# Kernel tuning notes

Hardware: AMD Instinct MI355X
Metric: run time of the kernel (lower is better)

The kernel has to match this reference:

```python
import jax, jax.numpy as jnp
import numpy as np

V, E, H, B, S, T = 32000, 32, 128, 128, 512, 16


def _gru_cell(x, h, w_ih, w_hh, b_ih, b_hh):
    # PyTorch GRU cell semantics.  x: [B, in], h: [B, H]
    gi = x @ w_ih.T + b_ih              # [B, 3H]
    gh = h @ w_hh.T + b_hh              # [B, 3H]
    i_r, i_z, i_n = jnp.split(gi, 3, axis=-1)
    h_r, h_z, h_n = jnp.split(gh, 3, axis=-1)
    r = jax.nn.sigmoid(i_r + h_r)
    z = jax.nn.sigmoid(i_z + h_z)
    n = jnp.tanh(i_n + r * h_n)
    return (1.0 - z) * n + z * h


def setup_inputs() -> dict:
    key = jax.random.key(0)
    ks = jax.random.split(key, 24)
    Hh = H // 2  # encoder hidden per direction = 64
    u = lambda k, shp, fan: jax.random.uniform(k, shp, jnp.float32, -1.0, 1.0) / np.sqrt(fan)
    inp = {
        'inputs': jax.random.randint(ks[0], (B, S), 0, V),
        'targets': jax.random.randint(ks[1], (B, T), 0, V),
        'emb': jax.random.normal(ks[2], (V, E), jnp.float32),
        # encoder forward direction
        'W_ih_f': u(ks[3], (3 * Hh, E), Hh), 'W_hh_f': u(ks[4], (3 * Hh, Hh), Hh),
        'b_ih_f': u(ks[5], (3 * Hh,), Hh), 'b_hh_f': u(ks[6], (3 * Hh,), Hh),
        # encoder backward direction
        'W_ih_b': u(ks[7], (3 * Hh, E), Hh), 'W_hh_b': u(ks[8], (3 * Hh, Hh), Hh),
        'b_ih_b': u(ks[9], (3 * Hh,), Hh), 'b_hh_b': u(ks[10], (3 * Hh,), Hh),
        # sGate linears
        'W1': u(ks[11], (H, H), H), 'b1': u(ks[12], (H,), H),
        'W2': u(ks[13], (H, H), H), 'b2': u(ks[14], (H,), H),
        # decoder GRU (input E + H = 160, hidden H)
        'W_ih_d': u(ks[15], (3 * H, E + H), H), 'W_hh_d': u(ks[16], (3 * H, H), H),
        'b_ih_d': u(ks[17], (3 * H,), H), 'b_hh_d': u(ks[18], (3 * H,), H),
        # decoder2vocab
        'W_out': u(ks[19], (V, H), H), 'b_out': u(ks[20], (V,), H),
    }
    return inp


def reference(inputs, targets, emb, W_ih_f, W_hh_f, b_ih_f, b_hh_f,
              W_ih_b, W_hh_b, b_ih_b, b_hh_b, W1, b1, W2, b2,
              W_ih_d, W_hh_d, b_ih_d, b_hh_d, W_out, b_out):
    Hh = H // 2
    # ---- encode ----
    embeds = emb[inputs]                       # [B, S, E]
    xs = embeds.transpose(1, 0, 2)             # [S, B, E] time-major
    h0 = jnp.zeros((inputs.shape[0], Hh), jnp.float32)

    def fwd_step(h, x):
        h = _gru_cell(x, h, W_ih_f, W_hh_f, b_ih_f, b_hh_f)
        return h, h

    def bwd_step(h, x):
        h = _gru_cell(x, h, W_ih_b, W_hh_b, b_ih_b, b_hh_b)
        return h, h

    h_f, outs_f = jax.lax.scan(fwd_step, h0, xs)
    h_b, outs_b = jax.lax.scan(bwd_step, h0, xs[::-1])
    outs_b = outs_b[::-1]
    outputs = jnp.concatenate([outs_f, outs_b], axis=-1).transpose(1, 0, 2)  # [B, S, H]
    sn = jnp.concatenate([h_f, h_b], axis=-1)[:, None, :]                    # [B, 1, H]
    sGate = jax.nn.sigmoid(outputs @ W1.T + b1 + sn @ W2.T + b2)
    enc_outs = outputs * sGate                                               # [B, S, H]

    # ---- attention decode (teacher forcing) ----
    h_dec0 = sn[:, 0, :]                       # [B, H]
    words = targets[:, :-1].T                  # [T-1, B]

    def dec_step(h, w):
        e = emb[w]                                                  # [B, E]
        alpha = jax.nn.softmax(jnp.einsum('bd,bsd->bs', h, enc_outs))
        c_t = jnp.einsum('bs,bsd->bd', alpha, enc_outs)             # [B, H]
        h = _gru_cell(jnp.concatenate([c_t, e], axis=-1), h,
                      W_ih_d, W_hh_d, b_ih_d, b_hh_d)
        return h, h @ W_out.T + b_out

    _, logits = jax.lax.scan(dec_step, h_dec0, words)  # [T-1, B, V]
    return logits.transpose(1, 0, 2)                   # [B, T-1, V]
```

## Files before the change

kernel.cpp:

```cpp
#include <hip/hip_runtime.h>
#include <hip/hip_bf16.h>


typedef unsigned short u16;
typedef unsigned int u32;
typedef __attribute__((ext_vector_type(8))) short short8;
typedef __attribute__((ext_vector_type(4))) float f32x4;

#define V_ 32000
#define E_ 32
#define H_ 128
#define B_ 128
#define S_ 512
#define TDEC 15

__device__ __forceinline__ float bfu(u32 u) {
    union { u32 i; float f; } v; v.i = u << 16; return v.f;
}
__device__ __forceinline__ u16 f2bf(float f) {
    union { float f; u32 i; } v; v.f = f;
    u32 x = v.i;
    u32 r = (x + 0x7fffu + ((x >> 16) & 1u)) >> 16;
    return (u16)r;
}
__device__ __forceinline__ void bf8_to_f(const uint4 p, float* f) {
    f[0] = bfu(p.x & 0xffffu); f[1] = bfu(p.x >> 16);
    f[2] = bfu(p.y & 0xffffu); f[3] = bfu(p.y >> 16);
    f[4] = bfu(p.z & 0xffffu); f[5] = bfu(p.z >> 16);
    f[6] = bfu(p.w & 0xffffu); f[7] = bfu(p.w >> 16);
}
__device__ __forceinline__ float sigm(float x) { return 1.f / (1.f + expf(-x)); }
__device__ __forceinline__ float sigm_fast(float x) { return 1.f / (1.f + __expf(-x)); }
__device__ __forceinline__ float tanh_fast(float x) {
    const float t = __expf(2.f * x);
    return (t - 1.f) / (t + 1.f);
}

__global__ __launch_bounds__(384) void gi_kernel(
    const int* __restrict__ inputs, const float* __restrict__ emb,
    const float* __restrict__ Wih_f, const float* __restrict__ bih_f,
    const float* __restrict__ bhh_f,
    const float* __restrict__ Wih_b, const float* __restrict__ bih_b,
    const float* __restrict__ bhh_b,
    float* __restrict__ gi)
{
    const int b  = blockIdx.x >> 3;
    const int s0 = (blockIdx.x & 7) << 6;
    const int tid = threadIdx.x;

    __shared__ float xs[64][E_];
    __shared__ int idx[64];
    if (tid < 64) idx[tid] = inputs[b * S_ + s0 + tid];
    __syncthreads();
    for (int i = tid; i < 64 * E_; i += 384) {
        xs[i >> 5][i & 31] = emb[(unsigned)idx[i >> 5] * E_ + (i & 31)];
    }
    __syncthreads();

    const int dir = (tid >= 192) ? 1 : 0;
    const int j = tid - dir * 192;
    const float* Wih = dir ? Wih_b : Wih_f;
    const float* bih = dir ? bih_b : bih_f;
    const float* bhh = dir ? bhh_b : bhh_f;

    float w[E_];
    #pragma unroll
    for (int k = 0; k < E_; k += 4)
        *(float4*)(w + k) = *(const float4*)(Wih + j * E_ + k);
    const float c = bih[j] + (j < 128 ? bhh[j] : 0.f);

    float* gout = gi + (((size_t)(dir * B_ + b)) * S_ + s0) * 192 + j;
    for (int r = 0; r < 64; r++) {
        const float4* xr = (const float4*)xs[r];
        float a0 = 0.f, a1 = 0.f, a2 = 0.f, a3 = 0.f;
        #pragma unroll
        for (int q = 0; q < E_ / 4; q++) {
            const float4 x = xr[q];
            a0 += x.x * w[4 * q + 0]; a1 += x.y * w[4 * q + 1];
            a2 += x.z * w[4 * q + 2]; a3 += x.w * w[4 * q + 3];
        }
        gout[(size_t)r * 192] = ((a0 + a1) + (a2 + a3)) + c;
    }
}

__global__ __launch_bounds__(192, 1) void encoder_kernel(
    const float* __restrict__ gi,
    const float* __restrict__ Whh_f, const float* __restrict__ bhh_f,
    const float* __restrict__ Whh_b, const float* __restrict__ bhh_b,
    u16* __restrict__ outputs, float* __restrict__ sn)
{
    const int tid = threadIdx.x;
    const int g = tid >> 6;
    const int j = tid & 63;
    const int b = blockIdx.x & 127;
    const int dir = blockIdx.x >> 7;

    const float* Whh = dir ? Whh_b : Whh_f;
    const float* bhh = dir ? bhh_b : bhh_f;

    f32x4 wv[16];
    {
        const f32x4* wr = (const f32x4*)(Whh + (g * 64 + j) * 64);
        #pragma unroll
        for (int k = 0; k < 16; k++) wv[k] = wr[k];
    }
    const float badd = (g == 2) ? bhh[128 + j] : 0.f;

    __shared__ __attribute__((aligned(16))) float hs[64];
    __shared__ float sg[4 * 64];
    if (tid < 64) hs[tid] = 0.f;
    float hmine = 0.f;

    const float* gp = gi + ((size_t)(dir * B_ + b)) * S_ * 192 + g * 64 + j;
    u16* orow = outputs + ((size_t)b * S_) * H_ + (dir << 6) + j;

    const int st = dir ? -1 : 1;
    int oc = dir ? (S_ - 1) : 0;

    float pa = gp[(long)oc * 192];
    float pb = gp[(long)(oc + st) * 192];

#define ENC_STEP(PCUR)                                                         \
    {                                                                          \
        __syncthreads();                  \
        f32x4 acc = {0.f, 0.f, 0.f, 0.f};                                      \
        _Pragma("unroll")                                                      \
        for (int q = 0; q < 16; q++)                                           \
            acc += *(const f32x4*)(hs + 4 * q) * wv[q];                        \
        const float d = (acc[0] + acc[1]) + (acc[2] + acc[3]);                 \
        if (g == 2) { sg[128 + j] = d + badd; sg[192 + j] = PCUR; }            \
        else        { sg[g * 64 + j] = d + PCUR; }                             \
        PCUR = gp[(long)(oc + 2 * st) * 192];           \
        __syncthreads();                                         \
        if (g == 0) {                                                          \
            const float r = sigm_fast(sg[j]);                                  \
            const float z = sigm_fast(sg[64 + j]);                             \
            const float n = tanh_fast(sg[192 + j] + r * sg[128 + j]);          \
            const float hn = n + z * (hmine - n);                              \
            hmine = hn;                                                        \
            hs[j] = hn;                                                        \
            orow[(long)oc * H_] = f2bf(hn);                                    \
        }                                                                      \
        oc += st;                                                              \
    }

    for (int s = 0; s < S_; s += 2) {
        ENC_STEP(pa)
        ENC_STEP(pb)
    }
#undef ENC_STEP

    if (g == 0) sn[(b << 7) + (dir << 6) + j] = hmine;
}

__global__ __launch_bounds__(128) void t2_kernel(
    const float* __restrict__ sn, const float* __restrict__ W2,
    const float* __restrict__ b2, float* __restrict__ t2)
{
    const int b = blockIdx.x, h = threadIdx.x;
    __shared__ float s_[H_];
    s_[h] = sn[b * H_ + h];
    __syncthreads();
    const float4* wr = (const float4*)(W2 + h * H_);
    float a0 = 0.f, a1 = 0.f, a2 = 0.f, a3 = 0.f;
    #pragma unroll 4
    for (int k = 0; k < H_ / 4; k++) {
        const float4 p = wr[k];
        a0 += s_[4 * k + 0] * p.x; a1 += s_[4 * k + 1] * p.y;
        a2 += s_[4 * k + 2] * p.z; a3 += s_[4 * k + 3] * p.w;
    }
    t2[b * H_ + h] = ((a0 + a1) + (a2 + a3)) + b2[h];
}

__global__ __launch_bounds__(256) void cvt_bf16_kernel(
    const float* __restrict__ src, u16* __restrict__ dst)
{
    const int i = (blockIdx.x * 256 + threadIdx.x) * 4;
    const float4 p = *(const float4*)(src + i);
    ushort4 q;
    q.x = f2bf(p.x); q.y = f2bf(p.y); q.z = f2bf(p.z); q.w = f2bf(p.w);
    *(ushort4*)(dst + i) = q;
}

__global__ __launch_bounds__(256) void gate_mfma_kernel(
    const u16* __restrict__ outputs, const u16* __restrict__ W1b,
    const float* __restrict__ b1, const float* __restrict__ t2,
    u16* __restrict__ enc)
{
    const int l = threadIdx.x & 63;
    const int w = threadIdx.x >> 6;
    const int tile_m = blockIdx.x * 64 + w * 16;
    const int row_a = tile_m + (l & 15);
    const int kb = (l >> 4) * 8;
    const int b = blockIdx.x >> 3;

    f32x4 acc[8] = {};
    #pragma unroll
    for (int kk = 0; kk < 4; kk++) {
        const int k0 = kk * 32 + kb;
        const short8 af = *(const short8*)(outputs + row_a * H_ + k0);
        #pragma unroll
        for (int i = 0; i < 8; i++) {
            const int n = i * 16 + (l & 15);
            const short8 bv = *(const short8*)(W1b + n * H_ + k0);
            acc[i] = __builtin_amdgcn_mfma_f32_16x16x32_bf16(af, bv, acc[i], 0, 0, 0);
        }
    }

    const int m_base = tile_m + (l >> 4) * 4;
    #pragma unroll
    for (int i = 0; i < 8; i++) {
        const int n = i * 16 + (l & 15);
        const float bias = b1[n] + t2[b * H_ + n];
        #pragma unroll
        for (int r = 0; r < 4; r++) {
            const int m = m_base + r;
            const float g = sigm_fast(acc[i][r] + bias);
            const float o = bfu(outputs[m * H_ + n]);
            enc[m * H_ + n] = f2bf(o * g);
        }
    }
}

__global__ __launch_bounds__(512) void decoder_kernel(
    const int* __restrict__ targets, const float* __restrict__ emb,
    const float* __restrict__ Wihd, const float* __restrict__ Whhd,
    const float* __restrict__ bihd, const float* __restrict__ bhhd,
    const u16* __restrict__ enc, const float* __restrict__ sn,
    u16* __restrict__ h_all)
{
    const int b = blockIdx.x;
    const int tid = threadIdx.x;
    const int lane = tid & 63;
    const int wid = tid >> 6;

    __shared__ __attribute__((aligned(16))) float h[H_];
    __shared__ float sc[S_];
    __shared__ float xv[H_ + E_];
    __shared__ float redm[8], reds[8];
    __shared__ float cpart[4][H_];
    __shared__ float sgi[3 * H_];
    __shared__ float sgh[3 * H_];

    if (tid < H_) h[tid] = sn[b * H_ + tid];
    __syncthreads();

    const u16* encb = enc + b * S_ * H_;

    for (int t = 0; t < TDEC; t++) {
        const int word = targets[b * 16 + t];

        const u16* row = encb + tid * H_;
        float a0 = 0.f, a1 = 0.f, a2 = 0.f, a3 = 0.f;
        #pragma unroll
        for (int k = 0; k < H_; k += 8) {
            uint4 p = *(const uint4*)(row + k);
            float f[8]; bf8_to_f(p, f);
            const f32x4 h0 = *(const f32x4*)(h + k);
            const f32x4 h1 = *(const f32x4*)(h + k + 4);
            a0 += h0[0] * f[0]; a1 += h0[1] * f[1];
            a2 += h0[2] * f[2]; a3 += h0[3] * f[3];
            a0 += h1[0] * f[4]; a1 += h1[1] * f[5];
            a2 += h1[2] * f[6]; a3 += h1[3] * f[7];
        }
        const float d = (a0 + a1) + (a2 + a3);

        float m = d;
        #pragma unroll
        for (int off = 32; off > 0; off >>= 1) m = fmaxf(m, __shfl_xor(m, off));
        if (lane == 0) redm[wid] = m;
        __syncthreads();
        float bm = redm[0];
        #pragma unroll
        for (int i = 1; i < 8; i++) bm = fmaxf(bm, redm[i]);
        const float e = expf(d - bm);
        float ssum = e;
        #pragma unroll
        for (int off = 32; off > 0; off >>= 1) ssum += __shfl_xor(ssum, off);
        if (lane == 0) reds[wid] = ssum;
        __syncthreads();
        float tot = reds[0];
        #pragma unroll
        for (int i = 1; i < 8; i++) tot += reds[i];
        sc[tid] = e * (1.f / tot);
        __syncthreads();

        {
            const int k = tid & 127;
            const int q = tid >> 7;
            const u16* basep = encb + (q * 128) * H_ + k;
            const float* al = sc + q * 128;
            float c0 = 0.f, c1 = 0.f, c2 = 0.f, c3 = 0.f;
            #pragma unroll 8
            for (int s = 0; s < 128; s += 4) {
                c0 += al[s + 0] * bfu(basep[(s + 0) * H_]);
                c1 += al[s + 1] * bfu(basep[(s + 1) * H_]);
                c2 += al[s + 2] * bfu(basep[(s + 2) * H_]);
                c3 += al[s + 3] * bfu(basep[(s + 3) * H_]);
            }
            cpart[q][k] = (c0 + c1) + (c2 + c3);
        }
        __syncthreads();
        if (tid < H_) xv[tid] = (cpart[0][tid] + cpart[1][tid]) + (cpart[2][tid] + cpart[3][tid]);
        else if (tid < H_ + E_) xv[tid] = emb[(unsigned)word * E_ + (tid - H_)];
        __syncthreads();

        if (tid < 3 * H_) {
            const int j = tid;
            const float4* wr = (const float4*)(Wihd + j * (H_ + E_));
            float g0 = 0.f, g1 = 0.f, g2 = 0.f, g3 = 0.f;
            #pragma unroll 8
            for (int k = 0; k < (H_ + E_) / 4; k++) {
                const float4 p = wr[k];
                g0 += xv[4 * k + 0] * p.x; g1 += xv[4 * k + 1] * p.y;
                g2 += xv[4 * k + 2] * p.z; g3 += xv[4 * k + 3] * p.w;
            }
            sgi[j] = ((g0 + g1) + (g2 + g3)) + bihd[j];

            const float4* hr = (const float4*)(Whhd + j * H_);
            float b0 = 0.f, b1_ = 0.f, b2_ = 0.f, b3 = 0.f;
            #pragma unroll 8
            for (int k = 0; k < H_ / 4; k++) {
                const float4 p = hr[k];
                b0  += h[4 * k + 0] * p.x; b1_ += h[4 * k + 1] * p.y;
                b2_ += h[4 * k + 2] * p.z; b3  += h[4 * k + 3] * p.w;
            }
            sgh[j] = ((b0 + b1_) + (b2_ + b3)) + bhhd[j];
        }
        __syncthreads();

        if (tid < H_) {
            const float r = sigm(sgi[tid] + sgh[tid]);
            const float z = sigm(sgi[H_ + tid] + sgh[H_ + tid]);
            const float n = tanhf(sgi[2 * H_ + tid] + r * sgh[2 * H_ + tid]);
            const float hn = (1.f - z) * n + z * h[tid];
            h[tid] = hn;
            h_all[(t * B_ + b) * H_ + tid] = f2bf(hn);
        }
        __syncthreads();
    }
}

__global__ __launch_bounds__(256) void logits_kernel(
    const u16* __restrict__ hall, const u16* __restrict__ Woutb,
    const float* __restrict__ bout, float* __restrict__ out)
{
    const int l = threadIdx.x & 63;
    const int w = threadIdx.x >> 6;
    const int tile_n = blockIdx.x * 64;
    const int tile_m = blockIdx.y * 64 + w * 16;

    f32x4 acc[4] = {};
    const int row_a = tile_m + (l & 15);
    const int kb = (l >> 4) * 8;

    #pragma unroll
    for (int kk = 0; kk < 4; kk++) {
        const int k0 = kk * 32 + kb;
        const short8 af = *(const short8*)(hall + row_a * H_ + k0);
        #pragma unroll
        for (int i = 0; i < 4; i++) {
            const int n = tile_n + i * 16 + (l & 15);
            const short8 bv = *(const short8*)(Woutb + n * H_ + k0);
            acc[i] = __builtin_amdgcn_mfma_f32_16x16x32_bf16(af, bv, acc[i], 0, 0, 0);
        }
    }

    const int m_base = tile_m + (l >> 4) * 4;
    #pragma unroll
    for (int i = 0; i < 4; i++) {
        const int n = tile_n + i * 16 + (l & 15);
        const float bias = bout[n];
        #pragma unroll
        for (int r = 0; r < 4; r++) {
            const int m = m_base + r;
            const int t = m >> 7;
            const int bb = m & 127;
            out[(size_t)(bb * TDEC + t) * V_ + n] = acc[i][r] + bias;
        }
    }
}

extern "C" void kernel_launch(void* const* d_in, const int* in_sizes, int n_in,
                              void* d_out, int out_size, void* d_ws, size_t ws_size,
                              hipStream_t stream) {
    const int*   inputs  = (const int*)d_in[0];
    const int*   targets = (const int*)d_in[1];
    const float* emb     = (const float*)d_in[2];
    const float* Wih_f   = (const float*)d_in[3];
    const float* Whh_f   = (const float*)d_in[4];
    const float* bih_f   = (const float*)d_in[5];
    const float* bhh_f   = (const float*)d_in[6];
    const float* Wih_b   = (const float*)d_in[7];
    const float* Whh_b   = (const float*)d_in[8];
    const float* bih_b   = (const float*)d_in[9];
    const float* bhh_b   = (const float*)d_in[10];
    const float* W1      = (const float*)d_in[11];
    const float* b1      = (const float*)d_in[12];
    const float* W2      = (const float*)d_in[13];
    const float* b2      = (const float*)d_in[14];
    const float* Wihd    = (const float*)d_in[15];
    const float* Whhd    = (const float*)d_in[16];
    const float* bihd    = (const float*)d_in[17];
    const float* bhhd    = (const float*)d_in[18];
    const float* Wout    = (const float*)d_in[19];
    const float* bout    = (const float*)d_in[20];
    float* out = (float*)d_out;

    u16*   outputs = (u16*)d_out;
    u16*   enc     = (u16*)((char*)d_out + 16777216);
    u16*   W1b     = (u16*)((char*)d_out + 33554432);
    float* gi      = (float*)((char*)d_out + 33619968);

    char* ws = (char*)d_ws;
    float* sn    = (float*)(ws);
    float* t2    = (float*)(ws + 65536);
    u16*   h_all = (u16*)(ws + 131072);
    u16*   Woutb = (u16*)(ws + 622592);

    gi_kernel<<<B_ * (S_ / 64), 384, 0, stream>>>(inputs, emb, Wih_f, bih_f, bhh_f,
                                                  Wih_b, bih_b, bhh_b, gi);
    encoder_kernel<<<256, 192, 0, stream>>>(gi, Whh_f, bhh_f, Whh_b, bhh_b, outputs, sn);
    t2_kernel<<<128, 128, 0, stream>>>(sn, W2, b2, t2);
    cvt_bf16_kernel<<<H_ * H_ / 1024, 256, 0, stream>>>(W1, W1b);
    cvt_bf16_kernel<<<V_ * H_ / 1024, 256, 0, stream>>>(Wout, Woutb);
    gate_mfma_kernel<<<B_ * S_ / 64, 256, 0, stream>>>(outputs, W1b, b1, t2, enc);
    decoder_kernel<<<128, 512, 0, stream>>>(targets, emb, Wihd, Whhd, bihd, bhhd,
                                            enc, sn, h_all);
    logits_kernel<<<dim3(500, 30), 256, 0, stream>>>(h_all, Woutb, bout, out);
}
```

Baseline: 972.0 us.

## Stage per-batch encoder outputs in swizzled LDS for decoder attention

```diff
diff --git a/kernel.cpp b/kernel.cpp
--- a/kernel.cpp
+++ b/kernel.cpp
@@ -222,7 +222,7 @@
     }
 }
 
-__global__ __launch_bounds__(512) void decoder_kernel(
+__global__ __launch_bounds__(512, 1) void decoder_kernel(
     const int* __restrict__ targets, const float* __restrict__ emb,
     const float* __restrict__ Wihd, const float* __restrict__ Whhd,
     const float* __restrict__ bihd, const float* __restrict__ bhhd,
@@ -234,36 +234,51 @@
     const int lane = tid & 63;
     const int wid = tid >> 6;
 
+    __shared__ __attribute__((aligned(16))) u16 enc_lds[S_ * H_];
     __shared__ __attribute__((aligned(16))) float h[H_];
     __shared__ float sc[S_];
     __shared__ float xv[H_ + E_];
     __shared__ float redm[8], reds[8];
-    __shared__ float cpart[4][H_];
+    __shared__ __attribute__((aligned(16))) float cpart[32][H_];
     __shared__ float sgi[3 * H_];
     __shared__ float sgh[3 * H_];
 
+    const u16* encb = enc + b * S_ * H_;
+
+    {
+        const int c = tid & 15;
+        const int sb = tid >> 4;
+        #pragma unroll
+        for (int i = 0; i < 16; i++) {
+            const int s = i * 32 + sb;
+            const uint4 p = *(const uint4*)(encb + s * H_ + c * 8);
+            *(uint4*)(enc_lds + s * H_ + ((c ^ (s & 15)) * 8)) = p;
+        }
+    }
     if (tid < H_) h[tid] = sn[b * H_ + tid];
     __syncthreads();
 
-    const u16* encb = enc + b * S_ * H_;
-
     for (int t = 0; t < TDEC; t++) {
         const int word = targets[b * 16 + t];
 
-        const u16* row = encb + tid * H_;
-        float a0 = 0.f, a1 = 0.f, a2 = 0.f, a3 = 0.f;
-        #pragma unroll
-        for (int k = 0; k < H_; k += 8) {
-            uint4 p = *(const uint4*)(row + k);
-            float f[8]; bf8_to_f(p, f);
-            const f32x4 h0 = *(const f32x4*)(h + k);
-            const f32x4 h1 = *(const f32x4*)(h + k + 4);
-            a0 += h0[0] * f[0]; a1 += h0[1] * f[1];
-            a2 += h0[2] * f[2]; a3 += h0[3] * f[3];
-            a0 += h1[0] * f[4]; a1 += h1[1] * f[5];
-            a2 += h1[2] * f[6]; a3 += h1[3] * f[7];
-        }
-        const float d = (a0 + a1) + (a2 + a3);
+        float d;
+        {
+            const int s = tid;
+            const int sx = s & 15;
+            float a0 = 0.f, a1 = 0.f, a2 = 0.f, a3 = 0.f;
+            #pragma unroll
+            for (int c = 0; c < 16; c++) {
+                const uint4 p = *(const uint4*)(enc_lds + s * H_ + ((c ^ sx) * 8));
+                float f[8]; bf8_to_f(p, f);
+                const f32x4 h0 = *(const f32x4*)(h + c * 8);
+                const f32x4 h1 = *(const f32x4*)(h + c * 8 + 4);
+                a0 += h0[0] * f[0]; a1 += h0[1] * f[1];
+                a2 += h0[2] * f[2]; a3 += h0[3] * f[3];
+                a0 += h1[0] * f[4]; a1 += h1[1] * f[5];
+                a2 += h1[2] * f[6]; a3 += h1[3] * f[7];
+            }
+            d = (a0 + a1) + (a2 + a3);
+        }
 
         float m = d;
         #pragma unroll
@@ -286,23 +301,33 @@
         __syncthreads();
 
         {
-            const int k = tid & 127;
-            const int q = tid >> 7;
-            const u16* basep = encb + (q * 128) * H_ + k;
-            const float* al = sc + q * 128;
-            float c0 = 0.f, c1 = 0.f, c2 = 0.f, c3 = 0.f;
-            #pragma unroll 8
-            for (int s = 0; s < 128; s += 4) {
-                c0 += al[s + 0] * bfu(basep[(s + 0) * H_]);
-                c1 += al[s + 1] * bfu(basep[(s + 1) * H_]);
-                c2 += al[s + 2] * bfu(basep[(s + 2) * H_]);
-                c3 += al[s + 3] * bfu(basep[(s + 3) * H_]);
+            const int c = tid & 15;
+            const int q = tid >> 4;
+            f32x4 ca = {0.f, 0.f, 0.f, 0.f}, cb = {0.f, 0.f, 0.f, 0.f};
+            #pragma unroll
+            for (int i = 0; i < 16; i++) {
+                const int s = q * 16 + i;
+                const float al = sc[s];
+                const uint4 p = *(const uint4*)(enc_lds + s * H_ + ((c ^ i) * 8));
+                float f[8]; bf8_to_f(p, f);
+                ca[0] += al * f[0]; ca[1] += al * f[1];
+                ca[2] += al * f[2]; ca[3] += al * f[3];
+                cb[0] += al * f[4]; cb[1] += al * f[5];
+                cb[2] += al * f[6]; cb[3] += al * f[7];
             }
-            cpart[q][k] = (c0 + c1) + (c2 + c3);
-        }
-        __syncthreads();
-        if (tid < H_) xv[tid] = (cpart[0][tid] + cpart[1][tid]) + (cpart[2][tid] + cpart[3][tid]);
-        else if (tid < H_ + E_) xv[tid] = emb[(unsigned)word * E_ + (tid - H_)];
+            *(f32x4*)(cpart[q] + c * 8) = ca;
+            *(f32x4*)(cpart[q] + c * 8 + 4) = cb;
+        }
+        __syncthreads();
+        if (tid < H_) {
+            float s0 = 0.f, s1 = 0.f, s2 = 0.f, s3 = 0.f;
+            #pragma unroll
+            for (int p = 0; p < 32; p += 4) {
+                s0 += cpart[p + 0][tid]; s1 += cpart[p + 1][tid];
+                s2 += cpart[p + 2][tid]; s3 += cpart[p + 3][tid];
+            }
+            xv[tid] = (s0 + s1) + (s2 + s3);
+        } else if (tid < H_ + E_) xv[tid] = emb[(unsigned)word * E_ + (tid - H_)];
         __syncthreads();
 
         if (tid < 3 * H_) {
```

New measurement: 949.4 us. 1.02x faster.
